# Kernel optimization log

Hardware: AMD Instinct MI355X
Metric: run time of the kernel (lower is better)

## Reference

```python
import jax, jax.numpy as jnp
import numpy as np

SPATIAL_SHAPES = [(128, 128), (64, 64), (32, 32), (16, 16)]
D_MODEL = 256
N_HEADS = 8
N_LEVELS = 4
N_POINTS = 4
HEAD_DIM = D_MODEL // N_HEADS
B = 2
LEN_Q = sum(h * w for h, w in SPATIAL_SHAPES)  # 21760
LEN_IN = LEN_Q


def setup_inputs() -> dict:
    key = jax.random.key(0)
    ks = jax.random.split(key, 11)
    s = 1.0 / np.sqrt(D_MODEL).astype(np.float32)
    query = jax.random.normal(ks[0], (B, LEN_Q, D_MODEL), jnp.float32)
    reference_points = jax.random.uniform(ks[1], (B, LEN_Q, N_LEVELS, 2), jnp.float32)
    input_flatten = jax.random.normal(ks[2], (B, LEN_IN, D_MODEL), jnp.float32)
    W_off = jax.random.normal(ks[3], (D_MODEL, N_HEADS * N_LEVELS * N_POINTS * 2), jnp.float32) * s
    b_off = jnp.zeros((N_HEADS * N_LEVELS * N_POINTS * 2,), jnp.float32)
    W_attn = jax.random.normal(ks[4], (D_MODEL, N_HEADS * N_LEVELS * N_POINTS), jnp.float32) * s
    b_attn = jnp.zeros((N_HEADS * N_LEVELS * N_POINTS,), jnp.float32)
    W_val = jax.random.normal(ks[5], (D_MODEL, D_MODEL), jnp.float32) * s
    b_val = jnp.zeros((D_MODEL,), jnp.float32)
    W_out = jax.random.normal(ks[6], (D_MODEL, D_MODEL), jnp.float32) * s
    b_out = jnp.zeros((D_MODEL,), jnp.float32)
    return {"query": query, "reference_points": reference_points, "input_flatten": input_flatten,
            "W_off": W_off, "b_off": b_off, "W_attn": W_attn, "b_attn": b_attn,
            "W_val": W_val, "b_val": b_val, "W_out": W_out, "b_out": b_out}


def _ms_deform_core(value, sampling_locations, attention_weights):
    # value: (B, H, Dh, N_total); sampling_locations: (B, Lq, H, L, P, 2) in [0,1]
    # attention_weights: (B, Lq, H, L*P)
    Bv, Hn, Dh, _ = value.shape
    Lq = sampling_locations.shape[1]
    P = sampling_locations.shape[4]
    BN = Bv * Hn
    grids = 2.0 * sampling_locations - 1.0
    splits = np.cumsum([h * w for h, w in SPATIAL_SHAPES])[:-1].tolist()
    value_list = jnp.split(value, splits, axis=3)
    sampled_levels = []
    for lid, (Hh, Ww) in enumerate(SPATIAL_SHAPES):
        # (BN, H*W, Dh)
        val_flat = jnp.transpose(value_list[lid].reshape(BN, Dh, Hh * Ww), (0, 2, 1))
        # (BN, Lq, P, 2)
        g = jnp.transpose(grids[:, :, :, lid, :, :], (0, 2, 1, 3, 4)).reshape(BN, Lq, P, 2)
        ix = ((g[..., 0] + 1.0) * Ww - 1.0) / 2.0
        iy = ((g[..., 1] + 1.0) * Hh - 1.0) / 2.0
        ix0 = jnp.floor(ix).astype(jnp.int32)
        iy0 = jnp.floor(iy).astype(jnp.int32)
        ix1 = ix0 + 1
        iy1 = iy0 + 1
        fx = (ix - ix0.astype(ix.dtype))[..., None]
        fy = (iy - iy0.astype(iy.dtype))[..., None]

        def valid(yy, xx):
            return ((xx >= 0) & (xx < Ww) & (yy >= 0) & (yy < Hh)).astype(val_flat.dtype)[..., None]

        def gather(yy, xx):
            idx = (jnp.clip(yy, 0, Hh - 1) * Ww + jnp.clip(xx, 0, Ww - 1)).reshape(BN, Lq * P)
            out = jnp.take_along_axis(val_flat, idx[:, :, None], axis=1)
            return out.reshape(BN, Lq, P, Dh)

        v00 = gather(iy0, ix0) * valid(iy0, ix0)
        v01 = gather(iy0, ix1) * valid(iy0, ix1)
        v10 = gather(iy1, ix0) * valid(iy1, ix0)
        v11 = gather(iy1, ix1) * valid(iy1, ix1)
        sampled = ((1 - fx) * (1 - fy) * v00 + fx * (1 - fy) * v01
                   + (1 - fx) * fy * v10 + fx * fy * v11)  # (BN, Lq, P, Dh)
        sampled_levels.append(jnp.transpose(sampled, (0, 3, 1, 2)))  # (BN, Dh, Lq, P)
    # (BN, Dh, Lq, L*P)
    sv = jnp.stack(sampled_levels, axis=-2).reshape(BN, Dh, Lq, N_LEVELS * P)
    attn = jnp.transpose(attention_weights, (0, 2, 1, 3)).reshape(BN, 1, Lq, N_LEVELS * P)
    out = jnp.sum(sv * attn, axis=-1)  # (BN, Dh, Lq)
    out = out.reshape(Bv, Hn * Dh, Lq)
    return jnp.transpose(out, (0, 2, 1))  # (B, Lq, d_model)


def reference(query, reference_points, input_flatten, W_off, b_off, W_attn, b_attn, W_val, b_val, W_out, b_out):
    Bq, Lq, _ = query.shape
    Len_in = input_flatten.shape[1]
    value = input_flatten @ W_val + b_val  # (B, Len_in, d_model)
    offsets = (query @ W_off + b_off).reshape(Bq, Lq, N_HEADS, N_LEVELS, N_POINTS, 2)
    attn = jax.nn.softmax((query @ W_attn + b_attn).reshape(Bq, Lq, N_HEADS, N_LEVELS * N_POINTS), axis=-1)
    # normalizer is (W, H) per level
    offset_normalizer = jnp.asarray([[w, h] for h, w in SPATIAL_SHAPES], dtype=query.dtype)
    sampling_locations = (reference_points[:, :, None, :, None, :]
                          + offsets / offset_normalizer[None, None, None, :, None, :])
    value = jnp.transpose(value, (0, 2, 1)).reshape(Bq, N_HEADS, HEAD_DIM, Len_in)
    out = _ms_deform_core(value, sampling_locations, attn)
    return out @ W_out + b_out
```

## Files before the change

### kernel.cpp

```cpp
#include <hip/hip_runtime.h>
#include <hip/hip_bf16.h>
#include <type_traits>

#define B_    2
#define LQ_   21760
#define LEN_  21760
#define DM    256
#define NH    8
#define NL    4
#define NP    4
#define HD    32

#define WS_VAL   0u
#define WS_QBF   22282240u
#define WS_INBF  44564480u
#define WS_OFF   66846720u
#define WS_ATTN  111411200u
#define WS_WT    133693440u

__device__ __forceinline__ unsigned short f2bf(float v) {
    __hip_bfloat16 h = __float2bfloat16(v);
    return *reinterpret_cast<unsigned short*>(&h);
}
__device__ __forceinline__ unsigned int pk2bf(float a, float b) {
    return (unsigned int)f2bf(a) | ((unsigned int)f2bf(b) << 16);
}

__global__ __launch_bounds__(256) void cvt_bf16(const float* __restrict__ x,
                                                unsigned short* __restrict__ y, int n4) {
    int i = blockIdx.x * 256 + threadIdx.x;
    if (i < n4) {
        float4 v = ((const float4*)x)[i];
        ushort4 u;
        u.x = f2bf(v.x); u.y = f2bf(v.y); u.z = f2bf(v.z); u.w = f2bf(v.w);
        ((ushort4*)y)[i] = u;
    }
}

__global__ __launch_bounds__(256) void wt_cvt(const float* __restrict__ W,
                                              unsigned short* __restrict__ Wt,
                                              int K, int N) {
    __shared__ float tile[16][17];
    const int n0 = blockIdx.x * 16, k0 = blockIdx.y * 16;
    const int tx = threadIdx.x & 15, ty = threadIdx.x >> 4;
    tile[ty][tx] = W[(size_t)(k0 + ty) * N + n0 + tx];
    __syncthreads();
    Wt[(size_t)(n0 + ty) * K + k0 + tx] = f2bf(tile[tx][ty]);
}

typedef __attribute__((ext_vector_type(8))) short bf16x8;
typedef __attribute__((ext_vector_type(4))) float f32x4;

template <typename TOut>
__global__ __launch_bounds__(256) void gemm_mfma(const unsigned short* __restrict__ A,
                                                 const unsigned short* __restrict__ Bt,
                                                 const float* __restrict__ bias,
                                                 TOut* __restrict__ C,
                                                 int M, int N, int K) {
    __shared__ unsigned short As[128 * 32];
    __shared__ unsigned short Bs[128 * 32];
    const int t = threadIdx.x;
    const int wv = t >> 6;
    const int ln = t & 63;
    const int m0 = blockIdx.x * 128;
    const int n0 = blockIdx.y * 128;
    const int wm = (wv & 1) * 64;
    const int wn = (wv >> 1) * 64;
    const int lrow = ln & 15;
    const int kq = ln >> 4;

    f32x4 acc[4][4] = {};

    for (int k0 = 0; k0 < K; k0 += 32) {
#pragma unroll
        for (int c = 0; c < 2; ++c) {
            const int o = c * 4096 + wv * 1024 + ln * 16;
            const int row = o >> 6;
            const int ke = (o & 63) >> 1;
            const unsigned short* ga = A + (size_t)(m0 + row) * K + k0 + ke;
            const unsigned short* gb = Bt + (size_t)(n0 + row) * K + k0 + ke;
            __builtin_amdgcn_global_load_lds(
                (const __attribute__((address_space(1))) void*)ga,
                (__attribute__((address_space(3))) void*)((char*)As + o), 16, 0, 0);
            __builtin_amdgcn_global_load_lds(
                (const __attribute__((address_space(1))) void*)gb,
                (__attribute__((address_space(3))) void*)((char*)Bs + o), 16, 0, 0);
        }
        __syncthreads();

        bf16x8 af[4], bfr[4];
#pragma unroll
        for (int i = 0; i < 4; ++i) {
            af[i]  = *(const bf16x8*)((char*)As + (wm + i * 16 + lrow) * 64 + kq * 16);
            bfr[i] = *(const bf16x8*)((char*)Bs + (wn + i * 16 + lrow) * 64 + kq * 16);
        }
#pragma unroll
        for (int i = 0; i < 4; ++i)
#pragma unroll
            for (int j = 0; j < 4; ++j)
                acc[i][j] = __builtin_amdgcn_mfma_f32_16x16x32_bf16(af[i], bfr[j], acc[i][j], 0, 0, 0);
        __syncthreads();
    }

#pragma unroll
    for (int j = 0; j < 4; ++j) {
        const int n = n0 + wn + j * 16 + lrow;
        const float bb = bias[n];
#pragma unroll
        for (int i = 0; i < 4; ++i) {
            const int mrow = m0 + wm + i * 16 + kq * 4;
#pragma unroll
            for (int r = 0; r < 4; ++r) {
                const float v = acc[i][j][r] + bb;
                if constexpr (std::is_same<TOut, float>::value) {
                    C[(size_t)(mrow + r) * N + n] = v;
                } else {
                    C[(size_t)(mrow + r) * N + n] = f2bf(v);
                }
            }
        }
    }
}

#define QB 8
__global__ __launch_bounds__(256) void msda_sample2(const unsigned short* __restrict__ value,
                                                    const float* __restrict__ offr,
                                                    const float* __restrict__ attnr,
                                                    const float* __restrict__ refp,
                                                    unsigned short* __restrict__ samp) {
    __shared__ float s_off[QB * 256];
    __shared__ float s_logit[QB * 128];
    __shared__ float s_ref[QB * 8];
    __shared__ float s_aw[QB * 8 * 16];
    __shared__ unsigned int s_pk[QB * 128 * 8];

    const int t = threadIdx.x;
    const int bq0 = blockIdx.x * QB;
    const int b = bq0 / LQ_;

    {
        const float4* so = (const float4*)(offr + (size_t)bq0 * 256);
        float4* dof = (float4*)s_off;
        dof[t] = so[t];
        dof[t + 256] = so[t + 256];
        ((float4*)s_logit)[t] = ((const float4*)(attnr + (size_t)bq0 * 128))[t];
        if (t < 16) ((float4*)s_ref)[t] = ((const float4*)(refp + (size_t)bq0 * 8))[t];
    }
    __syncthreads();

    if (t < 64) {
        const float* lg = s_logit + (t >> 3) * 128 + (t & 7) * 16;
        float m = -1e30f;
#pragma unroll
        for (int i = 0; i < 16; ++i) m = fmaxf(m, lg[i]);
        float e[16], s = 0.f;
#pragma unroll
        for (int i = 0; i < 16; ++i) { e[i] = __expf(lg[i] - m); s += e[i]; }
        const float inv = 1.f / s;
#pragma unroll
        for (int i = 0; i < 16; ++i) s_aw[t * 16 + i] = e[i] * inv;
    }
    __syncthreads();

    {
        const int Wls[4] = {128, 64, 32, 16};
        const int Hls[4] = {128, 64, 32, 16};
        const int st_[4] = {0, 16384, 20480, 21504};
#pragma unroll
        for (int ii = 0; ii < 4; ++ii) {
            const int s = t * 4 + ii;
            const int q = s >> 7;
            const int rest = s & 127;
            const int h = rest >> 4;
            const int l = (rest >> 2) & 3;
            const int Wl = Wls[l], Hl = Hls[l], base = st_[l];
            const float ix = s_ref[q * 8 + l * 2]     * (float)Wl - 0.5f + s_off[q * 256 + rest * 2];
            const float iy = s_ref[q * 8 + l * 2 + 1] * (float)Hl - 0.5f + s_off[q * 256 + rest * 2 + 1];
            const float fix = floorf(ix), fiy = floorf(iy);
            const int x0 = (int)fix, y0 = (int)fiy;
            const int x1 = x0 + 1, y1 = y0 + 1;
            const float fx = ix - fix, fy = iy - fiy;
            const bool vx0 = (x0 >= 0) & (x0 < Wl);
            const bool vx1 = (x1 >= 0) & (x1 < Wl);
            const bool vy0 = (y0 >= 0) & (y0 < Hl);
            const bool vy1 = (y1 >= 0) & (y1 < Hl);
            const int cx0 = min(max(x0, 0), Wl - 1);
            const int cx1 = min(max(x1, 0), Wl - 1);
            const int cy0 = min(max(y0, 0), Hl - 1);
            const int cy1 = min(max(y1, 0), Hl - 1);
            const float aw = s_aw[(q * 8 + h) * 16 + (rest & 15)];
            const float w00 = aw * (1.f - fx) * (1.f - fy) * (float)(vx0 && vy0);
            const float w01 = aw * fx * (1.f - fy)         * (float)(vx1 && vy0);
            const float w10 = aw * (1.f - fx) * fy         * (float)(vx0 && vy1);
            const float w11 = aw * fx * fy                 * (float)(vx1 && vy1);
            const int slot = (s * 8) ^ ((h & 3) << 3);
            s_pk[slot + 0] = base + cy0 * Wl + cx0;
            s_pk[slot + 1] = base + cy0 * Wl + cx1;
            s_pk[slot + 2] = base + cy1 * Wl + cx0;
            s_pk[slot + 3] = base + cy1 * Wl + cx1;
            s_pk[slot + 4] = __float_as_uint(w00);
            s_pk[slot + 5] = __float_as_uint(w01);
            s_pk[slot + 6] = __float_as_uint(w10);
            s_pk[slot + 7] = __float_as_uint(w11);
        }
    }
    __syncthreads();

    const int q = t >> 5;
    const int w = t & 31;
    const int h = w >> 2;
    const int dg = w & 3;
    const unsigned short* vbase = value + (size_t)b * LEN_ * DM + h * HD + dg * 8;

    float acc[8] = {0.f, 0.f, 0.f, 0.f, 0.f, 0.f, 0.f, 0.f};
    const int sbase = q * 128 + h * 16;
#pragma unroll
    for (int lp = 0; lp < 16; ++lp) {
        const int s = sbase + lp;
        const int slot = (s * 8) ^ ((h & 3) << 3);
        const uint4 iv = *(const uint4*)&s_pk[slot];
        const uint4 wv = *(const uint4*)&s_pk[slot + 4];
        const uint4 v00 = *(const uint4*)(vbase + (size_t)iv.x * DM);
        const uint4 v01 = *(const uint4*)(vbase + (size_t)iv.y * DM);
        const uint4 v10 = *(const uint4*)(vbase + (size_t)iv.z * DM);
        const uint4 v11 = *(const uint4*)(vbase + (size_t)iv.w * DM);
#pragma unroll
        for (int c = 0; c < 4; ++c) {
            const unsigned int u00 = (&v00.x)[c], u01 = (&v01.x)[c];
            const unsigned int u10 = (&v10.x)[c], u11 = (&v11.x)[c];
            const float w00 = __uint_as_float(wv.x), w01 = __uint_as_float(wv.y);
            const float w10 = __uint_as_float(wv.z), w11 = __uint_as_float(wv.w);
            float a0 = acc[c * 2], a1 = acc[c * 2 + 1];
            a0 = fmaf(w00, __uint_as_float(u00 << 16), a0);
            a1 = fmaf(w00, __uint_as_float(u00 & 0xffff0000u), a1);
            a0 = fmaf(w01, __uint_as_float(u01 << 16), a0);
            a1 = fmaf(w01, __uint_as_float(u01 & 0xffff0000u), a1);
            a0 = fmaf(w10, __uint_as_float(u10 << 16), a0);
            a1 = fmaf(w10, __uint_as_float(u10 & 0xffff0000u), a1);
            a0 = fmaf(w11, __uint_as_float(u11 << 16), a0);
            a1 = fmaf(w11, __uint_as_float(u11 & 0xffff0000u), a1);
            acc[c * 2] = a0;
            acc[c * 2 + 1] = a1;
        }
    }
    uint4 o;
    o.x = pk2bf(acc[0], acc[1]);
    o.y = pk2bf(acc[2], acc[3]);
    o.z = pk2bf(acc[4], acc[5]);
    o.w = pk2bf(acc[6], acc[7]);
    *(uint4*)(samp + (size_t)(bq0 + q) * 256 + h * HD + dg * 8) = o;
}

extern "C" void kernel_launch(void* const* d_in, const int* in_sizes, int n_in,
                              void* d_out, int out_size, void* d_ws, size_t ws_size,
                              hipStream_t stream) {
    const float* query  = (const float*)d_in[0];
    const float* refp   = (const float*)d_in[1];
    const float* inpf   = (const float*)d_in[2];
    const float* W_off  = (const float*)d_in[3];
    const float* b_off  = (const float*)d_in[4];
    const float* W_attn = (const float*)d_in[5];
    const float* b_attn = (const float*)d_in[6];
    const float* W_val  = (const float*)d_in[7];
    const float* b_val  = (const float*)d_in[8];
    const float* W_out  = (const float*)d_in[9];
    const float* b_out  = (const float*)d_in[10];
    float* out = (float*)d_out;

    char* ws = (char*)d_ws;
    unsigned short* val_bf  = (unsigned short*)(ws + WS_VAL);
    unsigned short* q_bf    = (unsigned short*)(ws + WS_QBF);
    unsigned short* in_bf   = (unsigned short*)(ws + WS_INBF);
    unsigned short* samp_bf = (unsigned short*)(ws + WS_INBF);
    float* offr  = (float*)(ws + WS_OFF);
    float* attnr = (float*)(ws + WS_ATTN);
    unsigned short* Wt_val  = (unsigned short*)(ws + WS_WT);
    unsigned short* Wt_off  = (unsigned short*)(ws + WS_WT + 131072);
    unsigned short* Wt_attn = (unsigned short*)(ws + WS_WT + 262144);
    unsigned short* Wt_out  = (unsigned short*)(ws + WS_WT + 327680);

    const int M = B_ * LQ_;
    const int n4 = M * DM / 4;

    cvt_bf16<<<dim3((n4 + 255) / 256), 256, 0, stream>>>(inpf, in_bf, n4);
    cvt_bf16<<<dim3((n4 + 255) / 256), 256, 0, stream>>>(query, q_bf, n4);
    wt_cvt<<<dim3(256 / 16, 256 / 16), 256, 0, stream>>>(W_val,  Wt_val,  256, 256);
    wt_cvt<<<dim3(256 / 16, 256 / 16), 256, 0, stream>>>(W_off,  Wt_off,  256, 256);
    wt_cvt<<<dim3(128 / 16, 256 / 16), 256, 0, stream>>>(W_attn, Wt_attn, 256, 128);
    wt_cvt<<<dim3(256 / 16, 256 / 16), 256, 0, stream>>>(W_out,  Wt_out,  256, 256);

    gemm_mfma<unsigned short><<<dim3(M / 128, 2), 256, 0, stream>>>(in_bf, Wt_val, b_val, val_bf, M, 256, 256);
    gemm_mfma<float><<<dim3(M / 128, 2), 256, 0, stream>>>(q_bf, Wt_off, b_off, offr, M, 256, 256);
    gemm_mfma<float><<<dim3(M / 128, 1), 256, 0, stream>>>(q_bf, Wt_attn, b_attn, attnr, M, 128, 256);

    msda_sample2<<<dim3(M / QB), 256, 0, stream>>>(val_bf, offr, attnr, refp, samp_bf);

    gemm_mfma<float><<<dim3(M / 128, 2), 256, 0, stream>>>(samp_bf, Wt_out, b_out, out, M, 256, 256);
}
```

Before: 333.1 us.

## Fuse offset/attention GEMMs, pack sampling metadata to 16-bit, add nontemporal loads and block remap

Merges the offset and attention-logit projections into one N=384 GEMM with split bias, so the query tile is read once and one launch is dropped. In the sampling kernel, corner indices are packed as 16-bit pairs and bilinear weights as bf16, which halves shared-memory traffic per sample and lets the buffers overlay in one smem region. It also remaps block order across 8 groups, uses a new XOR swizzle, and switches streaming loads and stores to nontemporal. Storing the weights in bf16 costs some precision in the sampling weights.

```diff
diff --git a/kernel.cpp b/kernel.cpp
--- a/kernel.cpp
+++ b/kernel.cpp
@@ -14,9 +14,12 @@
 #define WS_VAL   0u
 #define WS_QBF   22282240u
 #define WS_INBF  44564480u
-#define WS_OFF   66846720u
-#define WS_ATTN  111411200u
+#define WS_OA    66846720u
 #define WS_WT    133693440u
+
+typedef __attribute__((ext_vector_type(4))) float f32x4;
+typedef __attribute__((ext_vector_type(8))) short bf16x8;
+typedef __attribute__((ext_vector_type(4))) unsigned int u32x4;
 
 __device__ __forceinline__ unsigned short f2bf(float v) {
     __hip_bfloat16 h = __float2bfloat16(v);
@@ -30,7 +33,7 @@
                                                 unsigned short* __restrict__ y, int n4) {
     int i = blockIdx.x * 256 + threadIdx.x;
     if (i < n4) {
-        float4 v = ((const float4*)x)[i];
+        f32x4 v = __builtin_nontemporal_load((const f32x4*)x + i);
         ushort4 u;
         u.x = f2bf(v.x); u.y = f2bf(v.y); u.z = f2bf(v.z); u.w = f2bf(v.w);
         ((ushort4*)y)[i] = u;
@@ -48,13 +51,12 @@
     Wt[(size_t)(n0 + ty) * K + k0 + tx] = f2bf(tile[tx][ty]);
 }
 
-typedef __attribute__((ext_vector_type(8))) short bf16x8;
-typedef __attribute__((ext_vector_type(4))) float f32x4;
-
 template <typename TOut>
 __global__ __launch_bounds__(256) void gemm_mfma(const unsigned short* __restrict__ A,
                                                  const unsigned short* __restrict__ Bt,
                                                  const float* __restrict__ bias,
+                                                 const float* __restrict__ bias2,
+                                                 int nsplit,
                                                  TOut* __restrict__ C,
                                                  int M, int N, int K) {
     __shared__ unsigned short As[128 * 32];
@@ -105,7 +107,7 @@
 #pragma unroll
     for (int j = 0; j < 4; ++j) {
         const int n = n0 + wn + j * 16 + lrow;
-        const float bb = bias[n];
+        const float bb = (n < nsplit) ? bias[n] : bias2[n - nsplit];
 #pragma unroll
         for (int i = 0; i < 4; ++i) {
             const int mrow = m0 + wm + i * 16 + kq * 4;
@@ -123,28 +125,38 @@
 }
 
 #define QB 8
-__global__ __launch_bounds__(256) void msda_sample2(const unsigned short* __restrict__ value,
-                                                    const float* __restrict__ offr,
-                                                    const float* __restrict__ attnr,
+__global__ __launch_bounds__(256) void msda_sample3(const unsigned short* __restrict__ value,
+                                                    const float* __restrict__ oa,
                                                     const float* __restrict__ refp,
                                                     unsigned short* __restrict__ samp) {
-    __shared__ float s_off[QB * 256];
-    __shared__ float s_logit[QB * 128];
-    __shared__ float s_ref[QB * 8];
-    __shared__ float s_aw[QB * 8 * 16];
-    __shared__ unsigned int s_pk[QB * 128 * 8];
+    __shared__ char smem[16384 + 256];
+    unsigned int* s_pk   = (unsigned int*)smem;
+    float* s_off   = (float*)smem;
+    float* s_logit = (float*)(smem + 8192);
+    float* s_aw    = (float*)(smem + 12288);
+    float* s_ref   = (float*)(smem + 16384);
 
     const int t = threadIdx.x;
-    const int bq0 = blockIdx.x * QB;
+    const int j = blockIdx.x;
+    const int bq0 = ((j & 7) * 680 + (j >> 3)) * QB;
     const int b = bq0 / LQ_;
 
     {
-        const float4* so = (const float4*)(offr + (size_t)bq0 * 256);
-        float4* dof = (float4*)s_off;
-        dof[t] = so[t];
-        dof[t + 256] = so[t + 256];
-        ((float4*)s_logit)[t] = ((const float4*)(attnr + (size_t)bq0 * 128))[t];
-        if (t < 16) ((float4*)s_ref)[t] = ((const float4*)(refp + (size_t)bq0 * 8))[t];
+        const float* oab = oa + (size_t)bq0 * 384;
+#pragma unroll
+        for (int r = 0; r < 2; ++r) {
+            const int i = t + r * 256;
+            const int ql = i >> 6, c = i & 63;
+            ((f32x4*)s_off)[ql * 64 + c] =
+                __builtin_nontemporal_load((const f32x4*)(oab + (size_t)ql * 384) + c);
+        }
+        {
+            const int ql = t >> 5, c = t & 31;
+            ((f32x4*)s_logit)[ql * 32 + c] =
+                __builtin_nontemporal_load((const f32x4*)(oab + (size_t)ql * 384 + 256) + c);
+        }
+        if (t < 16)
+            ((f32x4*)s_ref)[t] = __builtin_nontemporal_load((const f32x4*)(refp + (size_t)bq0 * 8) + t);
     }
     __syncthreads();
 
@@ -162,6 +174,7 @@
     }
     __syncthreads();
 
+    unsigned int pk0[4], pk1[4], pk2[4], pk3[4];
     {
         const int Wls[4] = {128, 64, 32, 16};
         const int Hls[4] = {128, 64, 32, 16};
@@ -193,16 +206,21 @@
             const float w01 = aw * fx * (1.f - fy)         * (float)(vx1 && vy0);
             const float w10 = aw * (1.f - fx) * fy         * (float)(vx0 && vy1);
             const float w11 = aw * fx * fy                 * (float)(vx1 && vy1);
-            const int slot = (s * 8) ^ ((h & 3) << 3);
-            s_pk[slot + 0] = base + cy0 * Wl + cx0;
-            s_pk[slot + 1] = base + cy0 * Wl + cx1;
-            s_pk[slot + 2] = base + cy1 * Wl + cx0;
-            s_pk[slot + 3] = base + cy1 * Wl + cx1;
-            s_pk[slot + 4] = __float_as_uint(w00);
-            s_pk[slot + 5] = __float_as_uint(w01);
-            s_pk[slot + 6] = __float_as_uint(w10);
-            s_pk[slot + 7] = __float_as_uint(w11);
-        }
+            pk0[ii] = (unsigned int)(base + cy0 * Wl + cx0) | ((unsigned int)(base + cy0 * Wl + cx1) << 16);
+            pk1[ii] = (unsigned int)(base + cy1 * Wl + cx0) | ((unsigned int)(base + cy1 * Wl + cx1) << 16);
+            pk2[ii] = pk2bf(w00, w01);
+            pk3[ii] = pk2bf(w10, w11);
+        }
+    }
+    __syncthreads();
+
+#pragma unroll
+    for (int ii = 0; ii < 4; ++ii) {
+        const int s = t * 4 + ii;
+        const int q = s >> 7;
+        const int h = (s >> 4) & 7;
+        const int swz = ((h & 3) << 2) ^ ((((h >> 2) ^ (q & 1)) & 1) << 4);
+        *(uint4*)&s_pk[(s * 4) ^ swz] = make_uint4(pk0[ii], pk1[ii], pk2[ii], pk3[ii]);
     }
     __syncthreads();
 
@@ -210,26 +228,26 @@
     const int w = t & 31;
     const int h = w >> 2;
     const int dg = w & 3;
+    const int swz = ((h & 3) << 2) ^ ((((h >> 2) ^ (q & 1)) & 1) << 4);
     const unsigned short* vbase = value + (size_t)b * LEN_ * DM + h * HD + dg * 8;
 
     float acc[8] = {0.f, 0.f, 0.f, 0.f, 0.f, 0.f, 0.f, 0.f};
     const int sbase = q * 128 + h * 16;
 #pragma unroll
     for (int lp = 0; lp < 16; ++lp) {
-        const int s = sbase + lp;
-        const int slot = (s * 8) ^ ((h & 3) << 3);
-        const uint4 iv = *(const uint4*)&s_pk[slot];
-        const uint4 wv = *(const uint4*)&s_pk[slot + 4];
-        const uint4 v00 = *(const uint4*)(vbase + (size_t)iv.x * DM);
-        const uint4 v01 = *(const uint4*)(vbase + (size_t)iv.y * DM);
-        const uint4 v10 = *(const uint4*)(vbase + (size_t)iv.z * DM);
-        const uint4 v11 = *(const uint4*)(vbase + (size_t)iv.w * DM);
+        const uint4 pk = *(const uint4*)&s_pk[((sbase + lp) * 4) ^ swz];
+        const uint4 v00 = *(const uint4*)(vbase + (size_t)(pk.x & 0xffffu) * DM);
+        const uint4 v01 = *(const uint4*)(vbase + (size_t)(pk.x >> 16) * DM);
+        const uint4 v10 = *(const uint4*)(vbase + (size_t)(pk.y & 0xffffu) * DM);
+        const uint4 v11 = *(const uint4*)(vbase + (size_t)(pk.y >> 16) * DM);
+        const float w00 = __uint_as_float(pk.z << 16);
+        const float w01 = __uint_as_float(pk.z & 0xffff0000u);
+        const float w10 = __uint_as_float(pk.w << 16);
+        const float w11 = __uint_as_float(pk.w & 0xffff0000u);
 #pragma unroll
         for (int c = 0; c < 4; ++c) {
             const unsigned int u00 = (&v00.x)[c], u01 = (&v01.x)[c];
             const unsigned int u10 = (&v10.x)[c], u11 = (&v11.x)[c];
-            const float w00 = __uint_as_float(wv.x), w01 = __uint_as_float(wv.y);
-            const float w10 = __uint_as_float(wv.z), w11 = __uint_as_float(wv.w);
             float a0 = acc[c * 2], a1 = acc[c * 2 + 1];
             a0 = fmaf(w00, __uint_as_float(u00 << 16), a0);
             a1 = fmaf(w00, __uint_as_float(u00 & 0xffff0000u), a1);
@@ -243,12 +261,12 @@
             acc[c * 2 + 1] = a1;
         }
     }
-    uint4 o;
+    u32x4 o;
     o.x = pk2bf(acc[0], acc[1]);
     o.y = pk2bf(acc[2], acc[3]);
     o.z = pk2bf(acc[4], acc[5]);
     o.w = pk2bf(acc[6], acc[7]);
-    *(uint4*)(samp + (size_t)(bq0 + q) * 256 + h * HD + dg * 8) = o;
+    __builtin_nontemporal_store(o, (u32x4*)(samp + (size_t)(bq0 + q) * 256 + h * HD + dg * 8));
 }
 
 extern "C" void kernel_launch(void* const* d_in, const int* in_sizes, int n_in,
@@ -272,28 +290,28 @@
     unsigned short* q_bf    = (unsigned short*)(ws + WS_QBF);
     unsigned short* in_bf   = (unsigned short*)(ws + WS_INBF);
     unsigned short* samp_bf = (unsigned short*)(ws + WS_INBF);
-    float* offr  = (float*)(ws + WS_OFF);
-    float* attnr = (float*)(ws + WS_ATTN);
-    unsigned short* Wt_val  = (unsigned short*)(ws + WS_WT);
-    unsigned short* Wt_off  = (unsigned short*)(ws + WS_WT + 131072);
-    unsigned short* Wt_attn = (unsigned short*)(ws + WS_WT + 262144);
-    unsigned short* Wt_out  = (unsigned short*)(ws + WS_WT + 327680);
+    float* oa = (float*)(ws + WS_OA);
+    unsigned short* Wt_val = (unsigned short*)(ws + WS_WT);
+    unsigned short* Wt_oa  = (unsigned short*)(ws + WS_WT + 131072);
+    unsigned short* Wt_out = (unsigned short*)(ws + WS_WT + 327680);
 
     const int M = B_ * LQ_;
     const int n4 = M * DM / 4;
 
     cvt_bf16<<<dim3((n4 + 255) / 256), 256, 0, stream>>>(inpf, in_bf, n4);
     cvt_bf16<<<dim3((n4 + 255) / 256), 256, 0, stream>>>(query, q_bf, n4);
-    wt_cvt<<<dim3(256 / 16, 256 / 16), 256, 0, stream>>>(W_val,  Wt_val,  256, 256);
-    wt_cvt<<<dim3(256 / 16, 256 / 16), 256, 0, stream>>>(W_off,  Wt_off,  256, 256);
-    wt_cvt<<<dim3(128 / 16, 256 / 16), 256, 0, stream>>>(W_attn, Wt_attn, 256, 128);
-    wt_cvt<<<dim3(256 / 16, 256 / 16), 256, 0, stream>>>(W_out,  Wt_out,  256, 256);
-
-    gemm_mfma<unsigned short><<<dim3(M / 128, 2), 256, 0, stream>>>(in_bf, Wt_val, b_val, val_bf, M, 256, 256);
-    gemm_mfma<float><<<dim3(M / 128, 2), 256, 0, stream>>>(q_bf, Wt_off, b_off, offr, M, 256, 256);
-    gemm_mfma<float><<<dim3(M / 128, 1), 256, 0, stream>>>(q_bf, Wt_attn, b_attn, attnr, M, 128, 256);
-
-    msda_sample2<<<dim3(M / QB), 256, 0, stream>>>(val_bf, offr, attnr, refp, samp_bf);
-
-    gemm_mfma<float><<<dim3(M / 128, 2), 256, 0, stream>>>(samp_bf, Wt_out, b_out, out, M, 256, 256);
-}
+    wt_cvt<<<dim3(16, 16), 256, 0, stream>>>(W_val, Wt_val, 256, 256);
+    wt_cvt<<<dim3(16, 16), 256, 0, stream>>>(W_off, Wt_oa, 256, 256);
+    wt_cvt<<<dim3(8, 16), 256, 0, stream>>>(W_attn, Wt_oa + 256 * 256, 256, 128);
+    wt_cvt<<<dim3(16, 16), 256, 0, stream>>>(W_out, Wt_out, 256, 256);
+
+    gemm_mfma<unsigned short><<<dim3(M / 128, 2), 256, 0, stream>>>(
+        in_bf, Wt_val, b_val, b_val, 256, val_bf, M, 256, 256);
+    gemm_mfma<float><<<dim3(M / 128, 3), 256, 0, stream>>>(
+        q_bf, Wt_oa, b_off, b_attn, 256, oa, M, 384, 256);
+
+    msda_sample3<<<dim3(M / QB), 256, 0, stream>>>(val_bf, oa, refp, samp_bf);
+
+    gemm_mfma<float><<<dim3(M / 128, 2), 256, 0, stream>>>(
+        samp_bf, Wt_out, b_out, b_out, 256, out, M, 256, 256);
+}
```

Result: no change. 328.1 us (-1.5%).
